# Kernel tuning notes

Measured on AMD Instinct MI355X. Metric: run time of the kernel, lower is better.

## Reference

```python
import jax, jax.numpy as jnp
import numpy as np
import math

D_MODEL = 1024
NHEAD = 16
K_DIM = D_MODEL // NHEAD
B, S = 2, 2048

def setup_inputs() -> dict:
    key = jax.random.key(0)
    ks = jax.random.split(key, 12)
    sc = 1.0 / math.sqrt(D_MODEL)
    inp = {
        'query': jax.random.normal(ks[0], (B, S, D_MODEL), jnp.float32),
        'key':   jax.random.normal(ks[1], (B, S, D_MODEL), jnp.float32),
        'value': jax.random.normal(ks[2], (B, S, D_MODEL), jnp.float32),
        'Wq': jax.random.normal(ks[3], (D_MODEL, D_MODEL), jnp.float32) * sc,
        'bq': jnp.zeros((D_MODEL,), jnp.float32),
        'Wk': jax.random.normal(ks[4], (D_MODEL, D_MODEL), jnp.float32) * sc,
        'bk': jnp.zeros((D_MODEL,), jnp.float32),
        'Wv': jax.random.normal(ks[5], (D_MODEL, D_MODEL), jnp.float32) * sc,
        'bv': jnp.zeros((D_MODEL,), jnp.float32),
        'Wo': jax.random.normal(ks[6], (D_MODEL, D_MODEL), jnp.float32) * sc,
        'bo': jnp.zeros((D_MODEL,), jnp.float32),
    }
    return inp

def reference(query, key, value, Wq, bq, Wk, bk, Wv, bv, Wo, bo):
    b, s, _ = query.shape
    # Linear projections (torch Linear: x @ W.T + b), split into heads -> [b, h, s, d]
    Q = (query @ Wq.T + bq).reshape(b, s, NHEAD, K_DIM).transpose(0, 2, 1, 3)
    K = (key   @ Wk.T + bk).reshape(b, s, NHEAD, K_DIM).transpose(0, 2, 1, 3)
    V = (value @ Wv.T + bv).reshape(b, s, NHEAD, K_DIM).transpose(0, 2, 1, 3)
    scores = jnp.einsum('bhqd,bhkd->bhqk', Q, K) / math.sqrt(K_DIM)
    attn = jax.nn.softmax(scores, axis=-1)  # dropout = identity (eval)
    out = jnp.einsum('bhqk,bhkd->bhqd', attn, V)
    out = out.transpose(0, 2, 1, 3).reshape(b, s, D_MODEL)
    out = out @ Wo.T + bo
    return (out, attn)
```

## Files before the change

### kernel.cpp

```cpp
#include <hip/hip_runtime.h>
#include <hip/hip_bf16.h>
#include <stdint.h>

#define S_LEN 2048
#define NB 2
#define NH 16
#define DM 1024
#define KDIM 64
#define MTOK (NB*S_LEN)

typedef __attribute__((ext_vector_type(8))) short bf16x8;
typedef __attribute__((ext_vector_type(4))) float f32x4;
typedef __attribute__((ext_vector_type(4))) unsigned short u16x4;
typedef __attribute__((ext_vector_type(8))) unsigned short u16x8;

#define AS1 __attribute__((address_space(1)))
#define AS3 __attribute__((address_space(3)))

__device__ __forceinline__ unsigned short f2bf(float f) {
  unsigned int u = __builtin_bit_cast(unsigned int, f);
  return (unsigned short)((u + 0x7fffu + ((u >> 16) & 1u)) >> 16);
}
__device__ __forceinline__ f32x4 mfma16(bf16x8 a, bf16x8 b, f32x4 c) {
  return __builtin_amdgcn_mfma_f32_16x16x32_bf16(a, b, c, 0, 0, 0);
}

struct CvtArgs {
  const float* src[4];
  unsigned short* dst[4];
  int n[4];
};

__global__ __launch_bounds__(256) void cvt_f32_bf16(CvtArgs a) {
  const int seg = blockIdx.y;
  const float* __restrict__ s = a.src[seg];
  unsigned short* __restrict__ d = a.dst[seg];
  const int n4 = a.n[seg] >> 2;
  const int stride = gridDim.x * blockDim.x;
  for (int i = blockIdx.x * blockDim.x + threadIdx.x; i < n4; i += stride) {
    const float4 v = reinterpret_cast<const float4*>(s)[i];
    u16x4 o;
    o[0] = f2bf(v.x); o[1] = f2bf(v.y); o[2] = f2bf(v.z); o[3] = f2bf(v.w);
    reinterpret_cast<u16x4*>(d)[i] = o;
  }
}

struct GemmCvtArgs {
  const float* A[3];
  const unsigned short* W[3];
  const float* bias[3];
  void* dst[3];
  int mode[3];
};

__global__ __launch_bounds__(256, 2)
void gemm_cvt(GemmCvtArgs ga)
{
  __shared__ __align__(16) char smem[32768];

  const int z = blockIdx.z;
  const float* __restrict__ Af = ga.A[z];
  const unsigned short* __restrict__ Bw = ga.W[z];
  const float* __restrict__ bias = ga.bias[z];
  void* __restrict__ dst = ga.dst[z];
  const int mode = ga.mode[z];

  const int t = threadIdx.x;
  const int w = t >> 6, l = t & 63;
  const int g = l >> 4, cl = l & 15;

  const int L   = blockIdx.x + 8 * blockIdx.y;
  const int xcd = L & 7, ix = L >> 3;
  const int m0  = (xcd * 4 + (ix & 3)) * 128;
  const int n0  = (ix >> 2) * 128;

  const float* Ap = Af + (size_t)(m0 + (t >> 2)) * DM + (t & 3) * 8;
  const unsigned short* Bg = Bw + (size_t)(n0 + (t >> 2)) * DM + (t & 3) * 8;

  const int wm = (w >> 1) * 64, wn = (w & 1) * 64;

  f32x4 acc[4][4];
  #pragma unroll
  for (int i = 0; i < 4; ++i)
    #pragma unroll
    for (int j = 0; j < 4; ++j) acc[i][j] = 0.f;

  #define STAGE_B(step) do {                                                        \
    AS3 char* _buf = (AS3 char*)smem + ((step) & 1) * 16384;                         \
    __builtin_amdgcn_global_load_lds((const AS1 void*)(Bg + (step)*32),              \
                                     (AS3 void*)(_buf + 8192 + w*1024),   16, 0, 0); \
    __builtin_amdgcn_global_load_lds((const AS1 void*)(Bg + (step)*32 + 64*DM),      \
                                     (AS3 void*)(_buf + 12288 + w*1024),  16, 0, 0); \
  } while (0)

  #define ALOAD(step, ra, rb, rc, rd) do {                                           \
    const float* _p = Ap + (step) * 32;                                              \
    ra = *reinterpret_cast<const float4*>(_p);                                       \
    rb = *reinterpret_cast<const float4*>(_p + 4);                                   \
    const float* _q = _p + (size_t)64 * DM;                                          \
    rc = *reinterpret_cast<const float4*>(_q);                                       \
    rd = *reinterpret_cast<const float4*>(_q + 4);                                   \
  } while (0)

  #define AWRITE(step, ra, rb, rc, rd) do {                                          \
    AS3 char* _buf = (AS3 char*)smem + ((step) & 1) * 16384;                         \
    u16x8 _w0, _w1;                                                                  \
    _w0[0]=f2bf(ra.x); _w0[1]=f2bf(ra.y); _w0[2]=f2bf(ra.z); _w0[3]=f2bf(ra.w);      \
    _w0[4]=f2bf(rb.x); _w0[5]=f2bf(rb.y); _w0[6]=f2bf(rb.z); _w0[7]=f2bf(rb.w);      \
    _w1[0]=f2bf(rc.x); _w1[1]=f2bf(rc.y); _w1[2]=f2bf(rc.z); _w1[3]=f2bf(rc.w);      \
    _w1[4]=f2bf(rd.x); _w1[5]=f2bf(rd.y); _w1[6]=f2bf(rd.z); _w1[7]=f2bf(rd.w);      \
    *(AS3 u16x8*)(_buf + t*16) = _w0;                                                \
    *(AS3 u16x8*)(_buf + 4096 + t*16) = _w1;                                         \
  } while (0)

  #define COMPUTE(s) do {                                                            \
    const AS3 unsigned short* bufA =                                                 \
        (const AS3 unsigned short*)((AS3 char*)smem + ((s) & 1) * 16384);            \
    const AS3 unsigned short* bufB = bufA + 4096;                                    \
    bf16x8 af[4], bfv[4];                                                            \
    _Pragma("unroll")                                                                \
    for (int i = 0; i < 4; ++i)                                                      \
      af[i] = *(const AS3 bf16x8*)(bufA + (wm + 16*i + cl) * 32 + g*8);              \
    _Pragma("unroll")                                                                \
    for (int j = 0; j < 4; ++j)                                                      \
      bfv[j] = *(const AS3 bf16x8*)(bufB + (wn + 16*j + cl) * 32 + g*8);             \
    _Pragma("unroll")                                                                \
    for (int i = 0; i < 4; ++i)                                                      \
      _Pragma("unroll")                                                              \
      for (int j = 0; j < 4; ++j)                                                    \
        acc[i][j] = mfma16(af[i], bfv[j], acc[i][j]);                                \
  } while (0)

  #define GSEC(s, c0,c1,c2,c3, n0_,n1_,n2_,n3_) do {                                 \
    asm volatile("s_waitcnt lgkmcnt(0)" ::: "memory");                               \
    asm volatile("s_waitcnt vmcnt(4)" ::: "memory");                \
    __builtin_amdgcn_s_barrier();                                                    \
    __builtin_amdgcn_sched_barrier(0);                                               \
    STAGE_B((s) + 1);                                                                \
    COMPUTE(s);                                                                      \
    asm volatile("s_waitcnt vmcnt(2)" ::: "memory");              \
    AWRITE((s) + 1, c0, c1, c2, c3);                                                 \
    if ((s) + 2 < 32) ALOAD((s) + 2, n0_, n1_, n2_, n3_);                            \
  } while (0)

  float4 e0, e1, e2, e3, o0, o1, o2, o3;
  STAGE_B(0);
  ALOAD(0, e0, e1, e2, e3);
  ALOAD(1, o0, o1, o2, o3);
  asm volatile("s_waitcnt vmcnt(4)" ::: "memory");
  AWRITE(0, e0, e1, e2, e3);

  for (int sp = 0; sp < 15; ++sp) {
    GSEC(2*sp,     o0, o1, o2, o3,  e0, e1, e2, e3);
    GSEC(2*sp + 1, e0, e1, e2, e3,  o0, o1, o2, o3);
  }
  GSEC(30, o0, o1, o2, o3,  e0, e1, e2, e3);
  asm volatile("s_waitcnt lgkmcnt(0)" ::: "memory");
  asm volatile("s_waitcnt vmcnt(0)" ::: "memory");
  __builtin_amdgcn_s_barrier();
  __builtin_amdgcn_sched_barrier(0);
  COMPUTE(31);
  #undef GSEC
  #undef COMPUTE
  #undef AWRITE
  #undef ALOAD
  #undef STAGE_B

  if (mode == 1) {
    unsigned short* Cs = (unsigned short*)smem;
    __syncthreads();
    #pragma unroll
    for (int i = 0; i < 4; ++i) {
      #pragma unroll
      for (int j = 0; j < 4; ++j) {
        const int n = wn + 16*j + cl;
        const float bn = bias[n0 + n];
        const int u = (wm >> 2) + 4*i + g;
        const int us = u ^ (n & 31);
        u16x4 o;
        #pragma unroll
        for (int r = 0; r < 4; ++r) o[r] = f2bf(acc[i][j][r] + bn);
        *reinterpret_cast<u16x4*>(&Cs[n*128 + us*4]) = o;
      }
    }
    __syncthreads();
    {
      const int n = t >> 1, mh = (t & 1) * 64;
      const int ncol = n0 + n;
      const int h = ncol >> 6, d = ncol & (KDIM-1);
      const int b = m0 >> 11, s0 = m0 & (S_LEN-1);
      unsigned short* drow = (unsigned short*)dst
          + ((size_t)(b*NH + h)*KDIM + d)*S_LEN + s0 + mh;
      #pragma unroll
      for (int mm = 0; mm < 4; ++mm) {
        u16x4 v[4];
        #pragma unroll
        for (int k = 0; k < 4; ++k) {
          const int us = ((mh >> 2) + mm*4 + k) ^ (n & 31);
          v[k] = *reinterpret_cast<const u16x4*>(&Cs[n*128 + us*4]);
        }
        u16x8 w01, w23;
        #pragma unroll
        for (int e = 0; e < 4; ++e) {
          w01[e] = v[0][e]; w01[4+e] = v[1][e];
          w23[e] = v[2][e]; w23[4+e] = v[3][e];
        }
        *reinterpret_cast<u16x8*>(drow + mm*16)     = w01;
        *reinterpret_cast<u16x8*>(drow + mm*16 + 8) = w23;
      }
    }
  } else {
    #pragma unroll
    for (int i = 0; i < 4; ++i)
      #pragma unroll
      for (int j = 0; j < 4; ++j) {
        const int ncol = n0 + wn + 16*j + cl;
        const float bn = bias[ncol];
        #pragma unroll
        for (int r = 0; r < 4; ++r) {
          const int m = m0 + wm + 16*i + g*4 + r;
          const float v = acc[i][j][r] + bn;
          const int b = m >> 11, sR = m & (S_LEN-1);
          const int h = ncol >> 6, d = ncol & (KDIM-1);
          ((unsigned short*)dst)[((size_t)(b*NH + h)*S_LEN + sR)*KDIM + d] = f2bf(v);
        }
      }
  }
}

__global__ __launch_bounds__(256, 2)
void gemm_pipe(const unsigned short* __restrict__ A,
               const unsigned short* __restrict__ Bw,
               const float* __restrict__ bias,
               float* __restrict__ dst)
{
  __shared__ __align__(16) char smem[32768];

  const int t = threadIdx.x;
  const int w = t >> 6, l = t & 63;
  const int g = l >> 4, cl = l & 15;

  const int L   = blockIdx.x + 8 * blockIdx.y;
  const int xcd = L & 7, ix = L >> 3;
  const int m0  = (xcd * 4 + (ix & 3)) * 128;
  const int n0  = (ix >> 2) * 128;

  const unsigned short* Ag = A  + (size_t)(m0 + (t >> 2)) * DM + (t & 3) * 8;
  const unsigned short* Bg = Bw + (size_t)(n0 + (t >> 2)) * DM + (t & 3) * 8;

  const int wm = (w >> 1) * 64, wn = (w & 1) * 64;

  f32x4 acc[4][4];
  #pragma unroll
  for (int i = 0; i < 4; ++i)
    #pragma unroll
    for (int j = 0; j < 4; ++j) acc[i][j] = 0.f;

  #define STAGE(step) do {                                                          \
    AS3 char* _buf = (AS3 char*)smem + ((step) & 1) * 16384;                         \
    __builtin_amdgcn_global_load_lds((const AS1 void*)(Ag + (step)*32),              \
                                     (AS3 void*)(_buf + w*1024),          16, 0, 0); \
    __builtin_amdgcn_global_load_lds((const AS1 void*)(Ag + (step)*32 + 64*DM),      \
                                     (AS3 void*)(_buf + 4096 + w*1024),   16, 0, 0); \
    __builtin_amdgcn_global_load_lds((const AS1 void*)(Bg + (step)*32),              \
                                     (AS3 void*)(_buf + 8192 + w*1024),   16, 0, 0); \
    __builtin_amdgcn_global_load_lds((const AS1 void*)(Bg + (step)*32 + 64*DM),      \
                                     (AS3 void*)(_buf + 12288 + w*1024),  16, 0, 0); \
  } while (0)

  STAGE(0);
  for (int s = 0; s < 32; ++s) {
    if (s < 31) {
      STAGE(s + 1);
      asm volatile("s_waitcnt vmcnt(4)" ::: "memory");
    } else {
      asm volatile("s_waitcnt vmcnt(0)" ::: "memory");
    }
    __builtin_amdgcn_s_barrier();
    __builtin_amdgcn_sched_barrier(0);

    const AS3 unsigned short* bufA =
        (const AS3 unsigned short*)((AS3 char*)smem + (s & 1) * 16384);
    const AS3 unsigned short* bufB = bufA + 4096;
    bf16x8 af[4], bfv[4];
    #pragma unroll
    for (int i = 0; i < 4; ++i)
      af[i] = *(const AS3 bf16x8*)(bufA + (wm + 16*i + cl) * 32 + g*8);
    #pragma unroll
    for (int j = 0; j < 4; ++j)
      bfv[j] = *(const AS3 bf16x8*)(bufB + (wn + 16*j + cl) * 32 + g*8);
    #pragma unroll
    for (int i = 0; i < 4; ++i)
      #pragma unroll
      for (int j = 0; j < 4; ++j)
        acc[i][j] = mfma16(af[i], bfv[j], acc[i][j]);

    __builtin_amdgcn_sched_barrier(0);
    __builtin_amdgcn_s_barrier();
  }
  #undef STAGE

  #pragma unroll
  for (int i = 0; i < 4; ++i)
    #pragma unroll
    for (int j = 0; j < 4; ++j) {
      const int ncol = n0 + wn + 16*j + cl;
      const float bn = bias[ncol];
      #pragma unroll
      for (int r = 0; r < 4; ++r) {
        const int m = m0 + wm + 16*i + g*4 + r;
        dst[(size_t)m * DM + ncol] = acc[i][j][r] + bn;
      }
    }
}

__global__ __launch_bounds__(512, 4)
void attn_fused10(const unsigned short* __restrict__ Qh,
                  const unsigned short* __restrict__ Kh,
                  const unsigned short* __restrict__ Vt,
                  float* __restrict__ attn,
                  unsigned short* __restrict__ ctx)
{
  __shared__ __align__(16) char smem[75776];
  AS3 char* const KB = (AS3 char*)smem;
  AS3 char* const VB = (AS3 char*)smem + 32768;

  const int id  = blockIdx.x;
  const int swz = (id & 7) * 64 + (id >> 3);
  const int bh  = swz >> 4;
  const int q0  = (swz & 15) * 128;

  const int t = threadIdx.x, w = t >> 6, l = t & 63;
  const int g = l >> 4, cl = l & 15;
  AS3 char* const PBw = (AS3 char*)smem + 65536 + w * 1280;
  const int b = bh >> 4, h = bh & 15;

  const unsigned short* Qb = Qh + ((size_t)bh * S_LEN + q0 + w*16 + cl) * KDIM;
  const bf16x8 qf0 = *reinterpret_cast<const bf16x8*>(Qb + g*8);
  const bf16x8 qf1 = *reinterpret_cast<const bf16x8*>(Qb + 32 + g*8);

  const int rs = (w & 3)*8 + (l >> 3), js = l & 7;
  const unsigned short* pK = Kh + (size_t)bh*S_LEN*KDIM + (size_t)rs*KDIM
                                + (size_t)((js ^ (rs & 7)) * 8);
  const int dsv = (w & 3)*16 + (l >> 2), jv = l & 3;
  const int kst = (dsv & 3) ^ ((dsv >> 2) & 3);
  const unsigned short* pV = Vt + (size_t)bh*KDIM*S_LEN + (size_t)dsv*S_LEN
                                + (size_t)((jv ^ kst) * 8);

  const unsigned kvkey = (unsigned)((cl & 3) ^ ((cl >> 2) & 3));
  const unsigned koff0 = (unsigned)(cl*128 + ((g ^ (cl & 7)) << 4));
  const unsigned koff1 = (unsigned)(cl*128 + (((g + 4) ^ (cl & 7)) << 4));
  const float SC2 = 0.125f * 1.44269504f;

  #define STAGE_K(ch) do { int _b = (ch) & 7;                                               \
    if (w < 4) __builtin_amdgcn_global_load_lds((const AS1 void*)(pK + (size_t)(ch)*2048),  \
                   (AS3 void*)(KB + _b*4096 + (w&3)*1024), 16, 0, 0); } while (0)
  #define STAGE_KV(ch) do { int _b = (ch) & 7;                                              \
    if (w < 4) __builtin_amdgcn_global_load_lds((const AS1 void*)(pK + (size_t)(ch)*2048),  \
                   (AS3 void*)(KB + _b*4096 + (w&3)*1024), 16, 0, 0);                       \
    else       __builtin_amdgcn_global_load_lds((const AS1 void*)(pV + (size_t)(ch)*32),    \
                   (AS3 void*)(VB + _b*4096 + (w&3)*1024), 16, 0, 0); } while (0)

  float sa0 = 0.f, sa1 = 0.f, sa2 = 0.f, sa3 = 0.f;

  for (int i = 0; i < 6; ++i) STAGE_K(i);
  for (int k = 0; k < 32; ++k) {
    const int c = 2 * k;
    if (w < 4) asm volatile("s_waitcnt vmcnt(4)" ::: "memory");
    __builtin_amdgcn_s_barrier();
    __builtin_amdgcn_sched_barrier(0);
    STAGE_K(c + 6);
    STAGE_K(c + 7);
    #pragma unroll
    for (int cc = 0; cc < 2; ++cc) {
      AS3 const char* kb = KB + ((c + cc) & 7) * 4096;
      #pragma unroll
      for (int s = 0; s < 2; ++s) {
        const bf16x8 k0 = *(const AS3 bf16x8*)(kb + s*2048 + koff0);
        const bf16x8 k1 = *(const AS3 bf16x8*)(kb + s*2048 + koff1);
        f32x4 acc = {0.f, 0.f, 0.f, 0.f};
        acc = mfma16(k0, qf0, acc);
        acc = mfma16(k1, qf1, acc);
        sa0 += __builtin_exp2f(acc[0] * SC2);
        sa1 += __builtin_exp2f(acc[1] * SC2);
        sa2 += __builtin_exp2f(acc[2] * SC2);
        sa3 += __builtin_exp2f(acc[3] * SC2);
      }
    }
  }

  float ssum = (sa0 + sa1) + (sa2 + sa3);
  ssum += __shfl_xor(ssum, 16, 64);
  ssum += __shfl_xor(ssum, 32, 64);
  const float inv = 1.0f / ssum;

  __syncthreads();

  float* const arow = attn + ((size_t)bh * S_LEN + q0 + w*16 + cl) * S_LEN + g*4;
  f32x4 accP[4];
  #pragma unroll
  for (int dt = 0; dt < 4; ++dt) accP[dt] = 0.f;

  for (int i = 0; i < 6; ++i) STAGE_KV(i);
  for (int k = 0; k < 32; ++k) {
    const int c = 2 * k;
    if (k < 3) asm volatile("s_waitcnt vmcnt(4)"  ::: "memory");
    else       asm volatile("s_waitcnt vmcnt(16)" ::: "memory");
    __builtin_amdgcn_s_barrier();
    __builtin_amdgcn_sched_barrier(0);
    STAGE_KV(c + 6);
    STAGE_KV(c + 7);
    #pragma unroll
    for (int cc = 0; cc < 2; ++cc) {
      const int ch = c + cc;
      AS3 const char* kb = KB + (ch & 7) * 4096;
      AS3 const char* vb = VB + (ch & 7) * 4096;
      #pragma unroll
      for (int s = 0; s < 2; ++s) {
        const bf16x8 k0 = *(const AS3 bf16x8*)(kb + s*2048 + koff0);
        const bf16x8 k1 = *(const AS3 bf16x8*)(kb + s*2048 + koff1);
        f32x4 acc = {0.f, 0.f, 0.f, 0.f};
        acc = mfma16(k0, qf0, acc);
        acc = mfma16(k1, qf1, acc);
        f32x4 p;
        p[0] = __builtin_exp2f(acc[0] * SC2) * inv;
        p[1] = __builtin_exp2f(acc[1] * SC2) * inv;
        p[2] = __builtin_exp2f(acc[2] * SC2) * inv;
        p[3] = __builtin_exp2f(acc[3] * SC2) * inv;
        *reinterpret_cast<f32x4*>(arow + ch*32 + s*16) = p;
        u16x4 pb;
        pb[0] = f2bf(p[0]); pb[1] = f2bf(p[1]); pb[2] = f2bf(p[2]); pb[3] = f2bf(p[3]);
        *(AS3 u16x4*)(PBw + cl*80 + s*32 + g*8) = pb;
      }
      const bf16x8 ap = *(const AS3 bf16x8*)(PBw + cl*80 + g*16);
      #pragma unroll
      for (int dt = 0; dt < 4; ++dt) {
        const bf16x8 bv = *(const AS3 bf16x8*)(vb + (dt*16 + cl)*64 + ((g ^ kvkey) << 4));
        accP[dt] = mfma16(ap, bv, accP[dt]);
      }
    }
  }
  #undef STAGE_K
  #undef STAGE_KV

  #pragma unroll
  for (int r = 0; r < 4; ++r) {
    const size_t row = (size_t)(b * S_LEN + q0 + w*16 + g*4 + r);
    #pragma unroll
    for (int dt = 0; dt < 4; ++dt)
      ctx[row * DM + h * KDIM + dt*16 + cl] = f2bf(accP[dt][r]);
  }
}

extern "C" void kernel_launch(void* const* d_in, const int* in_sizes, int n_in,
                              void* d_out, int out_size, void* d_ws, size_t ws_size,
                              hipStream_t stream)
{
  const float* q_in = (const float*)d_in[0];
  const float* k_in = (const float*)d_in[1];
  const float* v_in = (const float*)d_in[2];
  const float* Wq   = (const float*)d_in[3];
  const float* bq   = (const float*)d_in[4];
  const float* Wk   = (const float*)d_in[5];
  const float* bk   = (const float*)d_in[6];
  const float* Wv   = (const float*)d_in[7];
  const float* bv   = (const float*)d_in[8];
  const float* Wo   = (const float*)d_in[9];
  const float* bo   = (const float*)d_in[10];

  unsigned short* wqbf = (unsigned short*)d_ws;
  unsigned short* wkbf = wqbf + (size_t)DM*DM;
  unsigned short* wvbf = wkbf + (size_t)DM*DM;
  unsigned short* wobf = wvbf + (size_t)DM*DM;
  unsigned short* Qhp  = wobf + (size_t)DM*DM;
  unsigned short* Khp  = Qhp  + (size_t)MTOK*DM;
  unsigned short* Vtp  = Khp  + (size_t)MTOK*DM;
  unsigned short* ctx  = Vtp  + (size_t)MTOK*DM;

  float* out0 = (float*)d_out;
  float* attn = out0 + (size_t)MTOK*DM;

  CvtArgs ca;
  ca.src[0] = Wq; ca.dst[0] = wqbf; ca.n[0] = DM*DM;
  ca.src[1] = Wk; ca.dst[1] = wkbf; ca.n[1] = DM*DM;
  ca.src[2] = Wv; ca.dst[2] = wvbf; ca.n[2] = DM*DM;
  ca.src[3] = Wo; ca.dst[3] = wobf; ca.n[3] = DM*DM;
  cvt_f32_bf16<<<dim3(64, 4), 256, 0, stream>>>(ca);

  GemmCvtArgs gq;
  gq.A[0] = q_in; gq.W[0] = wqbf; gq.bias[0] = bq; gq.dst[0] = Qhp; gq.mode[0] = 0;
  gq.A[1] = k_in; gq.W[1] = wkbf; gq.bias[1] = bk; gq.dst[1] = Khp; gq.mode[1] = 0;
  gq.A[2] = v_in; gq.W[2] = wvbf; gq.bias[2] = bv; gq.dst[2] = Vtp; gq.mode[2] = 1;
  gemm_cvt<<<dim3(8, 32, 3), 256, 0, stream>>>(gq);

  attn_fused10<<<dim3(512), 512, 0, stream>>>(Qhp, Khp, Vtp, attn, ctx);

  gemm_pipe<<<dim3(8, 32), 256, 0, stream>>>(ctx, wobf, bo, out0);
}
```

Before: 265.8 us.

## Process two query tiles per block, fusing second tile's row-sum into first PV pass

Each attention block now handles 256 query rows in two 128-row halves. The softmax denominator for the second half is computed inside the first half's P·V pass by reusing the same K fragments, which removes one standalone K-only sum pass per 128 rows. The cost is half as many blocks (256 on a large GPU), a lower launch-bounds occupancy hint, and more live registers.

New measurement: 302.6 us. +13.9%, slower.

```diff
diff --git a/kernel.cpp b/kernel.cpp
--- a/kernel.cpp
+++ b/kernel.cpp
@@ -314,8 +314,8 @@
     }
 }
 
-__global__ __launch_bounds__(512, 4)
-void attn_fused10(const unsigned short* __restrict__ Qh,
+__global__ __launch_bounds__(512, 2)
+void attn_fused12(const unsigned short* __restrict__ Qh,
                   const unsigned short* __restrict__ Kh,
                   const unsigned short* __restrict__ Vt,
                   float* __restrict__ attn,
@@ -326,18 +326,21 @@
   AS3 char* const VB = (AS3 char*)smem + 32768;
 
   const int id  = blockIdx.x;
-  const int swz = (id & 7) * 64 + (id >> 3);
-  const int bh  = swz >> 4;
-  const int q0  = (swz & 15) * 128;
+  const int swz = (id & 7) * 32 + (id >> 3);
+  const int bh  = swz >> 3;
+  const int q0  = (swz & 7) * 256;
 
   const int t = threadIdx.x, w = t >> 6, l = t & 63;
   const int g = l >> 4, cl = l & 15;
   AS3 char* const PBw = (AS3 char*)smem + 65536 + w * 1280;
   const int b = bh >> 4, h = bh & 15;
 
-  const unsigned short* Qb = Qh + ((size_t)bh * S_LEN + q0 + w*16 + cl) * KDIM;
-  const bf16x8 qf0 = *reinterpret_cast<const bf16x8*>(Qb + g*8);
-  const bf16x8 qf1 = *reinterpret_cast<const bf16x8*>(Qb + 32 + g*8);
+  const unsigned short* QbA = Qh + ((size_t)bh * S_LEN + q0 + w*16 + cl) * KDIM;
+  const bf16x8 qA0 = *reinterpret_cast<const bf16x8*>(QbA + g*8);
+  const bf16x8 qA1 = *reinterpret_cast<const bf16x8*>(QbA + 32 + g*8);
+  const unsigned short* QbB = QbA + (size_t)128 * KDIM;
+  const bf16x8 qB0 = *reinterpret_cast<const bf16x8*>(QbB + g*8);
+  const bf16x8 qB1 = *reinterpret_cast<const bf16x8*>(QbB + 32 + g*8);
 
   const int rs = (w & 3)*8 + (l >> 3), js = l & 7;
   const unsigned short* pK = Kh + (size_t)bh*S_LEN*KDIM + (size_t)rs*KDIM
@@ -379,8 +382,8 @@
         const bf16x8 k0 = *(const AS3 bf16x8*)(kb + s*2048 + koff0);
         const bf16x8 k1 = *(const AS3 bf16x8*)(kb + s*2048 + koff1);
         f32x4 acc = {0.f, 0.f, 0.f, 0.f};
-        acc = mfma16(k0, qf0, acc);
-        acc = mfma16(k1, qf1, acc);
+        acc = mfma16(k0, qA0, acc);
+        acc = mfma16(k1, qA1, acc);
         sa0 += __builtin_exp2f(acc[0] * SC2);
         sa1 += __builtin_exp2f(acc[1] * SC2);
         sa2 += __builtin_exp2f(acc[2] * SC2);
@@ -392,14 +395,15 @@
   float ssum = (sa0 + sa1) + (sa2 + sa3);
   ssum += __shfl_xor(ssum, 16, 64);
   ssum += __shfl_xor(ssum, 32, 64);
-  const float inv = 1.0f / ssum;
+  const float inv0 = 1.0f / ssum;
 
   __syncthreads();
 
-  float* const arow = attn + ((size_t)bh * S_LEN + q0 + w*16 + cl) * S_LEN + g*4;
+  float* const arow0 = attn + ((size_t)bh * S_LEN + q0 + w*16 + cl) * S_LEN + g*4;
   f32x4 accP[4];
   #pragma unroll
   for (int dt = 0; dt < 4; ++dt) accP[dt] = 0.f;
+  float sb0 = 0.f, sb1 = 0.f, sb2 = 0.f, sb3 = 0.f;
 
   for (int i = 0; i < 6; ++i) STAGE_KV(i);
   for (int k = 0; k < 32; ++k) {
@@ -420,17 +424,24 @@
         const bf16x8 k0 = *(const AS3 bf16x8*)(kb + s*2048 + koff0);
         const bf16x8 k1 = *(const AS3 bf16x8*)(kb + s*2048 + koff1);
         f32x4 acc = {0.f, 0.f, 0.f, 0.f};
-        acc = mfma16(k0, qf0, acc);
-        acc = mfma16(k1, qf1, acc);
+        acc = mfma16(k0, qA0, acc);
+        acc = mfma16(k1, qA1, acc);
         f32x4 p;
-        p[0] = __builtin_exp2f(acc[0] * SC2) * inv;
-        p[1] = __builtin_exp2f(acc[1] * SC2) * inv;
-        p[2] = __builtin_exp2f(acc[2] * SC2) * inv;
-        p[3] = __builtin_exp2f(acc[3] * SC2) * inv;
-        *reinterpret_cast<f32x4*>(arow + ch*32 + s*16) = p;
+        p[0] = __builtin_exp2f(acc[0] * SC2) * inv0;
+        p[1] = __builtin_exp2f(acc[1] * SC2) * inv0;
+        p[2] = __builtin_exp2f(acc[2] * SC2) * inv0;
+        p[3] = __builtin_exp2f(acc[3] * SC2) * inv0;
+        *reinterpret_cast<f32x4*>(arow0 + ch*32 + s*16) = p;
         u16x4 pb;
         pb[0] = f2bf(p[0]); pb[1] = f2bf(p[1]); pb[2] = f2bf(p[2]); pb[3] = f2bf(p[3]);
         *(AS3 u16x4*)(PBw + cl*80 + s*32 + g*8) = pb;
+        f32x4 acc1 = {0.f, 0.f, 0.f, 0.f};
+        acc1 = mfma16(k0, qB0, acc1);
+        acc1 = mfma16(k1, qB1, acc1);
+        sb0 += __builtin_exp2f(acc1[0] * SC2);
+        sb1 += __builtin_exp2f(acc1[1] * SC2);
+        sb2 += __builtin_exp2f(acc1[2] * SC2);
+        sb3 += __builtin_exp2f(acc1[3] * SC2);
       }
       const bf16x8 ap = *(const AS3 bf16x8*)(PBw + cl*80 + g*16);
       #pragma unroll
@@ -440,12 +451,71 @@
       }
     }
   }
+
+  #pragma unroll
+  for (int r = 0; r < 4; ++r) {
+    const size_t row = (size_t)(b * S_LEN + q0 + w*16 + g*4 + r);
+    #pragma unroll
+    for (int dt = 0; dt < 4; ++dt)
+      ctx[row * DM + h * KDIM + dt*16 + cl] = f2bf(accP[dt][r]);
+  }
+
+  float ssum1 = (sb0 + sb1) + (sb2 + sb3);
+  ssum1 += __shfl_xor(ssum1, 16, 64);
+  ssum1 += __shfl_xor(ssum1, 32, 64);
+  const float inv1 = 1.0f / ssum1;
+
+  __syncthreads();
+
+  float* const arow1 = attn + ((size_t)bh * S_LEN + q0 + 128 + w*16 + cl) * S_LEN + g*4;
+  #pragma unroll
+  for (int dt = 0; dt < 4; ++dt) accP[dt] = 0.f;
+
+  for (int i = 0; i < 6; ++i) STAGE_KV(i);
+  for (int k = 0; k < 32; ++k) {
+    const int c = 2 * k;
+    if (k < 3) asm volatile("s_waitcnt vmcnt(4)"  ::: "memory");
+    else       asm volatile("s_waitcnt vmcnt(16)" ::: "memory");
+    __builtin_amdgcn_s_barrier();
+    __builtin_amdgcn_sched_barrier(0);
+    STAGE_KV(c + 6);
+    STAGE_KV(c + 7);
+    #pragma unroll
+    for (int cc = 0; cc < 2; ++cc) {
+      const int ch = c + cc;
+      AS3 const char* kb = KB + (ch & 7) * 4096;
+      AS3 const char* vb = VB + (ch & 7) * 4096;
+      #pragma unroll
+      for (int s = 0; s < 2; ++s) {
+        const bf16x8 k0 = *(const AS3 bf16x8*)(kb + s*2048 + koff0);
+        const bf16x8 k1 = *(const AS3 bf16x8*)(kb + s*2048 + koff1);
+        f32x4 acc = {0.f, 0.f, 0.f, 0.f};
+        acc = mfma16(k0, qB0, acc);
+        acc = mfma16(k1, qB1, acc);
+        f32x4 p;
+        p[0] = __builtin_exp2f(acc[0] * SC2) * inv1;
+        p[1] = __builtin_exp2f(acc[1] * SC2) * inv1;
+        p[2] = __builtin_exp2f(acc[2] * SC2) * inv1;
+        p[3] = __builtin_exp2f(acc[3] * SC2) * inv1;
+        *reinterpret_cast<f32x4*>(arow1 + ch*32 + s*16) = p;
+        u16x4 pb;
+        pb[0] = f2bf(p[0]); pb[1] = f2bf(p[1]); pb[2] = f2bf(p[2]); pb[3] = f2bf(p[3]);
+        *(AS3 u16x4*)(PBw + cl*80 + s*32 + g*8) = pb;
+      }
+      const bf16x8 ap = *(const AS3 bf16x8*)(PBw + cl*80 + g*16);
+      #pragma unroll
+      for (int dt = 0; dt < 4; ++dt) {
+        const bf16x8 bv = *(const AS3 bf16x8*)(vb + (dt*16 + cl)*64 + ((g ^ kvkey) << 4));
+        accP[dt] = mfma16(ap, bv, accP[dt]);
+      }
+    }
+  }
   #undef STAGE_K
   #undef STAGE_KV
 
   #pragma unroll
   for (int r = 0; r < 4; ++r) {
-    const size_t row = (size_t)(b * S_LEN + q0 + w*16 + g*4 + r);
+    const size_t row = (size_t)(b * S_LEN + q0 + 128 + w*16 + g*4 + r);
     #pragma unroll
     for (int dt = 0; dt < 4; ++dt)
       ctx[row * DM + h * KDIM + dt*16 + cl] = f2bf(accP[dt][r]);
@@ -493,7 +563,7 @@
   gq.A[2] = v_in; gq.W[2] = wvbf; gq.bias[2] = bv; gq.dst[2] = Vtp; gq.mode[2] = 1;
   gemm_cvt<<<dim3(8, 32, 3), 256, 0, stream>>>(gq);
 
-  attn_fused10<<<dim3(512), 512, 0, stream>>>(Qhp, Khp, Vtp, attn, ctx);
+  attn_fused12<<<dim3(256), 512, 0, stream>>>(Qhp, Khp, Vtp, attn, ctx);
 
   gemm_pipe<<<dim3(8, 32), 256, 0, stream>>>(ctx, wobf, bo, out0);
 }
```
